# Performance work log

Hardware: AMD Instinct MI355X
Metric: run time of the kernel (lower is better)

Reference implementation:

```python
import jax, jax.numpy as jnp
import numpy as np

DIM = 1024
NUM_HEADS = 16
HEAD_DIM = DIM // NUM_HEADS


def setup_inputs() -> dict:
    key = jax.random.key(0)
    k_x, k_q, k_k, k_v, k_o = jax.random.split(key, 5)
    B, L = 2, 2048
    scale = 1.0 / np.sqrt(DIM)
    x_bld = jax.random.normal(k_x, (B, L, DIM), dtype=jnp.float32)
    # LinearGeneral kernels: (in_features, num_heads, head_dim) for q/k/v,
    # (num_heads, head_dim, out_features) for out. Init ~ lecun_normal-ish scale.
    Wq = jax.random.normal(k_q, (DIM, NUM_HEADS, HEAD_DIM), dtype=jnp.float32) * scale
    Wk = jax.random.normal(k_k, (DIM, NUM_HEADS, HEAD_DIM), dtype=jnp.float32) * scale
    Wv = jax.random.normal(k_v, (DIM, NUM_HEADS, HEAD_DIM), dtype=jnp.float32) * scale
    Wo = jax.random.normal(k_o, (NUM_HEADS, HEAD_DIM, DIM), dtype=jnp.float32) * scale
    return {"x_bld": x_bld, "Wq": Wq, "Wk": Wk, "Wv": Wv, "Wo": Wo}


def reference(x_bld, Wq, Wk, Wv, Wo) -> jnp.ndarray:
    # Projections: [B,L,D] x [D,H,hd] -> [B,L,H,hd]
    q_blhd = jnp.einsum('bld,dhk->blhk', x_bld, Wq)
    k_blhd = jnp.einsum('bld,dhk->blhk', x_bld, Wk)
    v_blhd = jnp.einsum('bld,dhk->blhk', x_bld, Wv)
    # Scores: [B,H,L,L]
    attn_bhll = jnp.einsum('bqhd,bkhd->bhqk', q_blhd, k_blhd)
    attn_bhll = attn_bhll / jnp.sqrt(jnp.asarray(HEAD_DIM, dtype=attn_bhll.dtype))
    L = x_bld.shape[1]
    qi = jnp.arange(L)[:, None]
    ki = jnp.arange(L)[None, :]
    mask_ll = ki <= qi  # causal, no window
    neg_inf = jnp.finfo(attn_bhll.dtype).min
    attn_bhll = jnp.where(mask_ll[None, None, :, :], attn_bhll, neg_inf)
    attn_bhll = jax.nn.softmax(attn_bhll, axis=-1)
    y_blhd = jnp.einsum('bhqk,bkhd->bqhd', attn_bhll, v_blhd)
    # Output projection: contract (H, hd) -> D
    return jnp.einsum('blhk,hkd->bld', y_blhd, Wo)
```

## Files before the change

kernel.cpp:

```cpp
#include <hip/hip_runtime.h>
#include <hip/hip_bf16.h>

typedef __hip_bfloat16 bf16;
typedef __attribute__((ext_vector_type(8))) short short8;
typedef __attribute__((ext_vector_type(4))) float f32x4;
typedef __attribute__((ext_vector_type(4))) unsigned int u32x4;

__device__ __forceinline__ float bfbits2f(unsigned short u) {
    return __uint_as_float(((unsigned int)u) << 16);
}
__device__ __forceinline__ unsigned short f2bfbits(float f) {
    union { float f; unsigned int u; } x;
    x.f = f;
    unsigned int r = x.u + 0x7FFFu + ((x.u >> 16) & 1u);
    return (unsigned short)(r >> 16);
}
__device__ __forceinline__ unsigned int pack_bf16x2(float lo, float hi) {
    unsigned int u0 = __float_as_uint(lo) + 0x8000u;
    unsigned int u1 = __float_as_uint(hi) + 0x8000u;
    return __builtin_amdgcn_perm(u1, u0, 0x07060302u);
}
__device__ __forceinline__ void async_copy16(const void* g, void* l) {
    __builtin_amdgcn_global_load_lds(
        (const __attribute__((address_space(1))) void*)g,
        (__attribute__((address_space(3))) void*)l, 16, 0, 0);
}
__device__ __forceinline__ bool sniff_bf16(const unsigned int* p, int lane) {
    unsigned int wd = p[lane];
    unsigned int e = (wd >> 7) & 0xFFu;
    return __popcll(__ballot(e >= 90u && e <= 150u)) > 40;
}

__global__ __launch_bounds__(256) void prep(
    const void* __restrict__ X, const void* __restrict__ W1,
    const void* __restrict__ W2, const void* __restrict__ W3,
    const void* __restrict__ W4, short* __restrict__ xb,
    short* __restrict__ O1, short* __restrict__ O2,
    short* __restrict__ O3, short* __restrict__ O4) {
    __shared__ float tbuf[32][33];
    const int bx = blockIdx.x;
    const int tid = threadIdx.x;
    const int lane = tid & 63;

    if (bx < 2048) {
        const bool isBf = sniff_bf16((const unsigned int*)X, lane);
        const int i = (bx * 256 + tid) * 8;
        if (isBf) {
            *(short8*)&xb[i] = *(const short8*)((const short*)X + i);
        } else {
            const float* xf = (const float*)X + i;
            float4 a = *(const float4*)xf;
            float4 b = *(const float4*)(xf + 4);
            short8 o;
            o[0] = (short)f2bfbits(a.x); o[1] = (short)f2bfbits(a.y);
            o[2] = (short)f2bfbits(a.z); o[3] = (short)f2bfbits(a.w);
            o[4] = (short)f2bfbits(b.x); o[5] = (short)f2bfbits(b.y);
            o[6] = (short)f2bfbits(b.z); o[7] = (short)f2bfbits(b.w);
            *(short8*)&xb[i] = o;
        }
    } else {
        const void* Ws[4] = {W1, W2, W3, W4};
        short* Os[4] = {O1, O2, O3, O4};
        const int t = bx - 2048;
        const int wsel = t >> 10;
        const int tile = t & 1023;
        const int bxt = tile & 31, byt = tile >> 5;
        const void* W = Ws[wsel];
        const bool isBf = sniff_bf16((const unsigned int*)W, lane);
        const float scale = (wsel == 0) ? 0.18033688f : 1.0f;
        short* O = Os[wsel];

        const int tx = tid & 31, ty = tid >> 5;
        const int gx = bxt * 32 + tx;
#pragma unroll
        for (int i = 0; i < 4; i++) {
            const int gy = byt * 32 + ty + i * 8;
            float v = isBf
                ? bfbits2f(((const unsigned short*)W)[(size_t)gy * 1024 + gx])
                : ((const float*)W)[(size_t)gy * 1024 + gx];
            tbuf[ty + i * 8][tx] = v * scale;
        }
        __syncthreads();
#pragma unroll
        for (int i = 0; i < 4; i++) {
            const int orow = bxt * 32 + ty + i * 8;
            const int ocol = byt * 32 + tx;
            O[(size_t)orow * 1024 + ocol] = (short)f2bfbits(tbuf[tx][ty + i * 8]);
        }
    }
}

template <int BN>
__global__ __launch_bounds__(256) void gemm_async(const short* __restrict__ A,
                                                  const short* __restrict__ Bt,
                                                  void* __restrict__ C,
                                                  const unsigned int* __restrict__ xdet,
                                                  short* __restrict__ VtGp,
                                                  int M, int N, int K) {
    __shared__ short As[2][128 * 32];
    __shared__ short Bs[2][BN * 32];
    constexpr int NI = BN / 32;

    const int tid = threadIdx.x;
    const int lane = tid & 63;
    const int wv = __builtin_amdgcn_readfirstlane(tid >> 6);
    const int quad = lane >> 4, l16 = lane & 15;
    const int wr = wv >> 1, wc = wv & 1;
    const int m0 = blockIdx.y * 128, n0 = blockIdx.x * BN;

    const int gr = lane >> 2;
    const int gc = ((lane & 3) ^ ((lane >> 3) & 3)) * 8;

    const f32x4 zero = {0.f, 0.f, 0.f, 0.f};
    f32x4 acc[4][NI];
#pragma unroll
    for (int mi = 0; mi < 4; mi++)
#pragma unroll
        for (int ni = 0; ni < NI; ni++) acc[mi][ni] = zero;

    const short* aptr[2];
    const short* bptr[BN / 64];
#pragma unroll
    for (int t = 0; t < 2; t++)
        aptr[t] = A + (size_t)(m0 + t * 64 + wv * 16 + gr) * K + gc;
#pragma unroll
    for (int t = 0; t < BN / 64; t++)
        bptr[t] = Bt + (size_t)(n0 + t * 64 + wv * 16 + gr) * K + gc;

#pragma unroll
    for (int t = 0; t < 2; t++) async_copy16(aptr[t], &As[0][(t * 64 + wv * 16) * 32]);
#pragma unroll
    for (int t = 0; t < BN / 64; t++) async_copy16(bptr[t], &Bs[0][(t * 64 + wv * 16) * 32]);

    const int ss = (quad ^ ((l16 >> 1) & 3)) * 8;

    for (int k0 = 0; k0 < K; k0 += 32) {
        const int cur = (k0 >> 5) & 1;
        __syncthreads();
        if (k0 + 32 < K) {
            const int nxt = cur ^ 1;
#pragma unroll
            for (int t = 0; t < 2; t++)
                async_copy16(aptr[t] + k0 + 32, &As[nxt][(t * 64 + wv * 16) * 32]);
#pragma unroll
            for (int t = 0; t < BN / 64; t++)
                async_copy16(bptr[t] + k0 + 32, &Bs[nxt][(t * 64 + wv * 16) * 32]);
        }

        short8 af[4], bfv[NI];
#pragma unroll
        for (int mi = 0; mi < 4; mi++)
            af[mi] = *(const short8*)&As[cur][(wr * 64 + mi * 16 + l16) * 32 + ss];
#pragma unroll
        for (int ni = 0; ni < NI; ni++)
            bfv[ni] = *(const short8*)&Bs[cur][(wc * (BN / 2) + ni * 16 + l16) * 32 + ss];
#pragma unroll
        for (int mi = 0; mi < 4; mi++)
#pragma unroll
            for (int ni = 0; ni < NI; ni++)
                acc[mi][ni] = __builtin_amdgcn_mfma_f32_16x16x32_bf16(
                    af[mi], bfv[ni], acc[mi][ni], 0, 0, 0);
    }

    if (VtGp != nullptr && n0 >= 2048) {
        unsigned short* Vw = (unsigned short*)VtGp;
#pragma unroll
        for (int mi = 0; mi < 4; mi++)
#pragma unroll
            for (int ni = 0; ni < NI; ni++)
#pragma unroll
                for (int r = 0; r < 4; r++) {
                    const int row = m0 + wr * 64 + mi * 16 + quad * 4 + r;
                    const int col = n0 + wc * (BN / 2) + ni * 16 + l16;
                    const int vcol = col - 2048;
                    const int hh = vcol >> 6, d = vcol & 63;
                    const int bb = row >> 11, lloc = row & 2047;
                    const int pl = (lloc & ~31) + 2 * (lloc & 15) + ((lloc >> 4) & 1);
                    Vw[((size_t)(bb * 16 + hh) * 64 + d) * 2048 + pl] =
                        f2bfbits(acc[mi][ni][r]);
                }
        return;
    }

    bool outBf = true;
    if (xdet) outBf = sniff_bf16(xdet, lane);
    if (outBf) {
        unsigned short* Cb = (unsigned short*)C;
#pragma unroll
        for (int mi = 0; mi < 4; mi++)
#pragma unroll
            for (int ni = 0; ni < NI; ni++)
#pragma unroll
                for (int r = 0; r < 4; r++) {
                    const int row = m0 + wr * 64 + mi * 16 + quad * 4 + r;
                    const int col = n0 + wc * (BN / 2) + ni * 16 + l16;
                    Cb[(size_t)row * N + col] = f2bfbits(acc[mi][ni][r]);
                }
    } else {
        float* Cf = (float*)C;
#pragma unroll
        for (int mi = 0; mi < 4; mi++)
#pragma unroll
            for (int ni = 0; ni < NI; ni++)
#pragma unroll
                for (int r = 0; r < 4; r++) {
                    const int row = m0 + wr * 64 + mi * 16 + quad * 4 + r;
                    const int col = n0 + wc * (BN / 2) + ni * 16 + l16;
                    Cf[(size_t)row * N + col] = acc[mi][ni][r];
                }
    }
}

__global__ __launch_bounds__(256) void attn_mfma9(
    const short* __restrict__ qkv, const short* __restrict__ VtG,
    short* __restrict__ Yg, short* __restrict__ Opart, float* __restrict__ ml) {
    __shared__ short Ks[2][64 * 64];
    __shared__ short Vt[2][64 * 64];
    __shared__ float scr[16][68];
    __shared__ float lred[2][64];

    const int tid = threadIdx.x;
    const int lane = tid & 63;
    const int wv = __builtin_amdgcn_readfirstlane(tid >> 6);
    const int wvq = wv >> 1, wvk = wv & 1;
    const int quad = lane >> 4, l16 = lane & 15;
    const int bh = blockIdx.x;
    const int b = bh >> 4, h = bh & 15;

    int qb, seg, S;
    const int slot = blockIdx.y;
    if (slot < 64)      { qb = 31 - (slot >> 2); seg = slot & 3; S = 4; }
    else if (slot < 80) { const int t2 = slot - 64; qb = 15 - (t2 >> 1); seg = t2 & 1; S = 2; }
    else                { qb = 87 - slot; seg = 0; S = 1; }

    const int ns = qb + 1;
    const int sb0 = seg * ns / S;
    const int sb1 = (seg + 1) * ns / S;

    const int rr = lane >> 3;
    const int scol = ((lane & 7) ^ rr) * 8;

    const short* kptr[2];
    const short* vptr[2];
    short* kdst[2];
    short* vdst[2];
#pragma unroll
    for (int i = 0; i < 2; i++) {
        const int u = wv * 2 + i;
        kptr[i] = qkv + (size_t)(b * 2048 + sb0 * 64 + u * 8 + rr) * 3072 + 1024 +
                  h * 64 + scol;
        kdst[i] = &Ks[0][(u * 8) * 64];
        vptr[i] = VtG + ((size_t)bh * 64 + u * 8 + rr) * 2048 + sb0 * 64 + scol;
        vdst[i] = &Vt[0][(u * 8) * 64];
    }
    const int bufoff = 64 * 64;
    const int buf0 = sb0 & 1;

#pragma unroll
    for (int i = 0; i < 2; i++) {
        async_copy16(kptr[i], kdst[i] + buf0 * bufoff);
        async_copy16(vptr[i], vdst[i] + buf0 * bufoff);
        kptr[i] += 64 * 3072;
        vptr[i] += 64;
    }
    short8 qf[2][2];
    {
        const short* qbase = qkv + (size_t)(b * 2048 + qb * 64 + wvq * 32 + l16) * 3072 +
                             h * 64 + quad * 8;
#pragma unroll
        for (int qt = 0; qt < 2; qt++)
#pragma unroll
            for (int hf = 0; hf < 2; hf++)
                qf[qt][hf] = *(const short8*)(qbase + qt * 16 * 3072 + hf * 32);
    }
    __syncthreads();

    const int sl = (quad ^ (l16 & 7)) * 8;

    const f32x4 minit = {-17.3123405f, -17.3123405f, -17.3123405f, -17.3123405f};
    f32x4 O[2][4];
#pragma unroll
    for (int qt = 0; qt < 2; qt++)
#pragma unroll
        for (int dt = 0; dt < 4; dt++) O[qt][dt] = {0.f, 0.f, 0.f, 0.f};
    float lp[2] = {0.f, 0.f};
    const int keyA0 = wvk * 32 + quad * 4;

    for (int sb = sb0; sb < sb1; sb++) {
        const int cur = sb & 1;
        if (sb != sb0) __syncthreads();
        if (sb + 1 < sb1) {
            const int nxt = cur ^ 1;
#pragma unroll
            for (int i = 0; i < 2; i++) {
                async_copy16(kptr[i], kdst[i] + nxt * bufoff);
                async_copy16(vptr[i], vdst[i] + nxt * bufoff);
                kptr[i] += 64 * 3072;
                vptr[i] += 64;
            }
        }
        const short* Kc = &Ks[cur][0];
        const short* Vc = &Vt[cur][0];

        short8 kf[2][2], vf[4];
#pragma unroll
        for (int kt = 0; kt < 2; kt++)
#pragma unroll
            for (int hf = 0; hf < 2; hf++)
                kf[kt][hf] = *(const short8*)
                    &Kc[(wvk * 32 + kt * 16 + l16) * 64 + (sl ^ (hf << 5))];
#pragma unroll
        for (int dt = 0; dt < 4; dt++)
            vf[dt] = *(const short8*)
                &Vc[(dt * 16 + l16) * 64 + (sl ^ (wvk << 5))];

#pragma unroll
        for (int qt = 0; qt < 2; qt++) {
            f32x4 sA = __builtin_amdgcn_mfma_f32_16x16x32_bf16(kf[0][0], qf[qt][0], minit, 0, 0, 0);
            sA = __builtin_amdgcn_mfma_f32_16x16x32_bf16(kf[0][1], qf[qt][1], sA, 0, 0, 0);
            f32x4 sB = __builtin_amdgcn_mfma_f32_16x16x32_bf16(kf[1][0], qf[qt][0], minit, 0, 0, 0);
            sB = __builtin_amdgcn_mfma_f32_16x16x32_bf16(kf[1][1], qf[qt][1], sB, 0, 0, 0);
            if (sb == qb) {
                const int qcol = wvq * 32 + qt * 16 + l16;
#pragma unroll
                for (int r = 0; r < 4; r++) {
                    if (keyA0 + r > qcol) sA[r] = -1e30f;
                    if (keyA0 + 16 + r > qcol) sB[r] = -1e30f;
                }
            }
            union { u32x4 u; short8 s; } pa;
#pragma unroll
            for (int t = 0; t < 4; t++) {
                sA[t] = __builtin_amdgcn_exp2f(sA[t]);
                sB[t] = __builtin_amdgcn_exp2f(sB[t]);
                lp[qt] += sA[t] + sB[t];
                pa.u[t] = pack_bf16x2(sA[t], sB[t]);
            }
#pragma unroll
            for (int dt = 0; dt < 4; dt++)
                O[qt][dt] = __builtin_amdgcn_mfma_f32_16x16x32_bf16(
                    pa.s, vf[dt], O[qt][dt], 0, 0, 0);
        }
    }

#pragma unroll
    for (int qt = 0; qt < 2; qt++) {
        float v = lp[qt];
        v += __shfl_xor(v, 16);
        v += __shfl_xor(v, 32);
        if (quad == 0) lred[wvk][wvq * 32 + qt * 16 + l16] = v;
    }

#pragma unroll
    for (int g = 0; g < 2; g++)
#pragma unroll
        for (int qt = 0; qt < 2; qt++) {
            __syncthreads();
            if (wvq == g && wvk == 1) {
#pragma unroll
                for (int dt = 0; dt < 4; dt++)
#pragma unroll
                    for (int r = 0; r < 4; r++)
                        scr[quad * 4 + r][dt * 16 + l16] = O[qt][dt][r];
            }
            __syncthreads();
            if (wvq == g && wvk == 0) {
#pragma unroll
                for (int dt = 0; dt < 4; dt++)
#pragma unroll
                    for (int r = 0; r < 4; r++)
                        O[qt][dt][r] += scr[quad * 4 + r][dt * 16 + l16];
            }
        }

    if (wvk == 0) {
        if (S == 1) {
#pragma unroll
            for (int qt = 0; qt < 2; qt++)
#pragma unroll
                for (int r = 0; r < 4; r++) {
                    const int q = wvq * 32 + qt * 16 + quad * 4 + r;
                    const float inv = 1.f / (lred[0][q] + lred[1][q]);
#pragma unroll
                    for (int dt = 0; dt < 4; dt++)
                        Yg[(size_t)(b * 2048 + qb * 64 + q) * 1024 + h * 64 +
                           dt * 16 + l16] = (short)f2bfbits(O[qt][dt][r] * inv);
                }
        } else {
            const int qidx = qb - 8;
            const int base = ((seg * 32 + bh) * 24 + qidx) * 64;
#pragma unroll
            for (int qt = 0; qt < 2; qt++)
#pragma unroll
                for (int r = 0; r < 4; r++) {
                    const int q = wvq * 32 + qt * 16 + quad * 4 + r;
#pragma unroll
                    for (int dt = 0; dt < 4; dt++)
                        Opart[(size_t)(base + q) * 64 + dt * 16 + l16] =
                            (short)f2bfbits(O[qt][dt][r]);
                    if (l16 == 0) ml[base + q] = lred[0][q] + lred[1][q];
                }
        }
    }
}

__global__ __launch_bounds__(256) void attn_combine6(
    const short* __restrict__ Opart, const float* __restrict__ ml,
    short* __restrict__ Yg) {
    const int qb = 8 + blockIdx.x;
    const int bh = blockIdx.y;
    const int b = bh >> 4, h = bh & 15;
    const int S = (qb >= 16) ? 4 : 2;
    const int qidx = qb - 8;
    const int tid = threadIdx.x;
    const int q = tid >> 2;
    const int d0 = (tid & 3) * 16;

    float a0[8] = {}, a1[8] = {};
    float lsum = 0.f;
    for (int s = 0; s < S; s++) {
        const int idx = ((s * 32 + bh) * 24 + qidx) * 64 + q;
        lsum += ml[idx];
        const short* p = Opart + (size_t)idx * 64 + d0;
        short8 x0 = *(const short8*)p;
        short8 x1 = *(const short8*)(p + 8);
#pragma unroll
        for (int t = 0; t < 8; t++) {
            a0[t] += bfbits2f((unsigned short)x0[t]);
            a1[t] += bfbits2f((unsigned short)x1[t]);
        }
    }
    const float inv = 1.f / lsum;
    short8 o0, o1;
#pragma unroll
    for (int t = 0; t < 8; t++) {
        o0[t] = (short)f2bfbits(a0[t] * inv);
        o1[t] = (short)f2bfbits(a1[t] * inv);
    }
    short* yp = Yg + (size_t)(b * 2048 + qb * 64 + q) * 1024 + h * 64 + d0;
    *(short8*)yp = o0;
    *(short8*)(yp + 8) = o1;
}

extern "C" void kernel_launch(void* const* d_in, const int* in_sizes, int n_in,
                              void* d_out, int out_size, void* d_ws, size_t ws_size,
                              hipStream_t stream) {
    const int M = 2 * 2048;
    const int D = 1024;

    char* w = (char*)d_ws;
    short* xb  = (short*)w;
    short* WqT = (short*)(w + (8u << 20));
    short* WkT = WqT + (1u << 20);
    short* WvT = WkT + (1u << 20);
    short* WoT = WvT + (1u << 20);
    short* qkv = WoT + (1u << 20);
    short* VtG = qkv + (size_t)M * 3072;
    short* Opart = VtG + (size_t)2048 * 2048;
    float* mlp = (float*)(Opart + (size_t)4 * 32 * 24 * 64 * 64);
    short* y = xb;

    prep<<<6144, 256, 0, stream>>>(d_in[0], d_in[1], d_in[2], d_in[3], d_in[4],
                                   xb, WqT, WkT, WvT, WoT);

    gemm_async<128><<<dim3(3072 / 128, M / 128), 256, 0, stream>>>(
        xb, WqT, qkv, nullptr, VtG, M, 3072, D);

    attn_mfma9<<<dim3(32, 88), 256, 0, stream>>>(qkv, VtG, y, Opart, mlp);
    attn_combine6<<<dim3(24, 32), 256, 0, stream>>>(Opart, mlp, y);

    gemm_async<64><<<dim3(D / 64, M / 128), 256, 0, stream>>>(
        y, WoT, d_out, (const unsigned int*)d_in[0], nullptr, M, D, D);
}
```

Before: 180.8 us.

## Enlarge attention query tile to 128 rows, one 32-query slice per wave

The attention kernel now processes 128-query blocks, and each of the four waves owns 32 queries across all 64 keys of a tile. Previously the waves split along keys and had to reduce partial outputs through shared memory. This doubles reuse of each K/V tile loaded into LDS and removes the cross-wave O reduction with its barriers. It also adds per-wave causal masking over two diagonal tiles, s_setprio around the PV MFMAs, and a launch-bounds occupancy hint. The trade-off is fewer blocks (44 slots instead of 88) and some wasted masked work on diagonal tiles.

```diff
diff --git a/kernel.cpp b/kernel.cpp
--- a/kernel.cpp
+++ b/kernel.cpp
@@ -211,29 +211,27 @@
     }
 }
 
-__global__ __launch_bounds__(256) void attn_mfma9(
+__global__ __launch_bounds__(256, 4) void attn_mfma12(
     const short* __restrict__ qkv, const short* __restrict__ VtG,
     short* __restrict__ Yg, short* __restrict__ Opart, float* __restrict__ ml) {
     __shared__ short Ks[2][64 * 64];
     __shared__ short Vt[2][64 * 64];
-    __shared__ float scr[16][68];
-    __shared__ float lred[2][64];
+    __shared__ float lred[4][32];
 
     const int tid = threadIdx.x;
     const int lane = tid & 63;
     const int wv = __builtin_amdgcn_readfirstlane(tid >> 6);
-    const int wvq = wv >> 1, wvk = wv & 1;
     const int quad = lane >> 4, l16 = lane & 15;
     const int bh = blockIdx.x;
     const int b = bh >> 4, h = bh & 15;
 
-    int qb, seg, S;
+    int qbb, seg, S;
     const int slot = blockIdx.y;
-    if (slot < 64)      { qb = 31 - (slot >> 2); seg = slot & 3; S = 4; }
-    else if (slot < 80) { const int t2 = slot - 64; qb = 15 - (t2 >> 1); seg = t2 & 1; S = 2; }
-    else                { qb = 87 - slot; seg = 0; S = 1; }
-
-    const int ns = qb + 1;
+    if (slot < 32)      { qbb = 15 - (slot >> 2); seg = slot & 3; S = 4; }
+    else if (slot < 40) { const int t2 = slot - 32; qbb = 7 - (t2 >> 1); seg = t2 & 1; S = 2; }
+    else                { qbb = 43 - slot; seg = 0; S = 1; }
+
+    const int ns = 2 * qbb + 2;
     const int sb0 = seg * ns / S;
     const int sb1 = (seg + 1) * ns / S;
 
@@ -265,8 +263,8 @@
     }
     short8 qf[2][2];
     {
-        const short* qbase = qkv + (size_t)(b * 2048 + qb * 64 + wvq * 32 + l16) * 3072 +
-                             h * 64 + quad * 8;
+        const short* qbase = qkv +
+            (size_t)(b * 2048 + qbb * 128 + wv * 32 + l16) * 3072 + h * 64 + quad * 8;
 #pragma unroll
         for (int qt = 0; qt < 2; qt++)
 #pragma unroll
@@ -284,7 +282,7 @@
 #pragma unroll
         for (int dt = 0; dt < 4; dt++) O[qt][dt] = {0.f, 0.f, 0.f, 0.f};
     float lp[2] = {0.f, 0.f};
-    const int keyA0 = wvk * 32 + quad * 4;
+    const int qmin = qbb * 128 + wv * 32;
 
     for (int sb = sb0; sb < sb1; sb++) {
         const int cur = sb & 1;
@@ -301,45 +299,53 @@
         }
         const short* Kc = &Ks[cur][0];
         const short* Vc = &Vt[cur][0];
-
-        short8 kf[2][2], vf[4];
-#pragma unroll
-        for (int kt = 0; kt < 2; kt++)
-#pragma unroll
-            for (int hf = 0; hf < 2; hf++)
-                kf[kt][hf] = *(const short8*)
-                    &Kc[(wvk * 32 + kt * 16 + l16) * 64 + (sl ^ (hf << 5))];
-#pragma unroll
-        for (int dt = 0; dt < 4; dt++)
-            vf[dt] = *(const short8*)
-                &Vc[(dt * 16 + l16) * 64 + (sl ^ (wvk << 5))];
-
-#pragma unroll
-        for (int qt = 0; qt < 2; qt++) {
-            f32x4 sA = __builtin_amdgcn_mfma_f32_16x16x32_bf16(kf[0][0], qf[qt][0], minit, 0, 0, 0);
-            sA = __builtin_amdgcn_mfma_f32_16x16x32_bf16(kf[0][1], qf[qt][1], sA, 0, 0, 0);
-            f32x4 sB = __builtin_amdgcn_mfma_f32_16x16x32_bf16(kf[1][0], qf[qt][0], minit, 0, 0, 0);
-            sB = __builtin_amdgcn_mfma_f32_16x16x32_bf16(kf[1][1], qf[qt][1], sB, 0, 0, 0);
-            if (sb == qb) {
-                const int qcol = wvq * 32 + qt * 16 + l16;
-#pragma unroll
-                for (int r = 0; r < 4; r++) {
-                    if (keyA0 + r > qcol) sA[r] = -1e30f;
-                    if (keyA0 + 16 + r > qcol) sB[r] = -1e30f;
+        const bool needmask = (sb * 64 + 63 > qmin);
+
+#pragma unroll
+        for (int c = 0; c < 2; c++) {
+            short8 kf0[2], kf1[2], vf[4];
+#pragma unroll
+            for (int hf = 0; hf < 2; hf++) {
+                kf0[hf] = *(const short8*)
+                    &Kc[((2 * c) * 16 + l16) * 64 + (sl ^ (hf << 5))];
+                kf1[hf] = *(const short8*)
+                    &Kc[((2 * c + 1) * 16 + l16) * 64 + (sl ^ (hf << 5))];
+            }
+#pragma unroll
+            for (int dt = 0; dt < 4; dt++)
+                vf[dt] = *(const short8*)
+                    &Vc[(dt * 16 + l16) * 64 + (sl ^ (c << 5))];
+
+#pragma unroll
+            for (int qt = 0; qt < 2; qt++) {
+                f32x4 sA = __builtin_amdgcn_mfma_f32_16x16x32_bf16(kf0[0], qf[qt][0], minit, 0, 0, 0);
+                sA = __builtin_amdgcn_mfma_f32_16x16x32_bf16(kf0[1], qf[qt][1], sA, 0, 0, 0);
+                f32x4 sB = __builtin_amdgcn_mfma_f32_16x16x32_bf16(kf1[0], qf[qt][0], minit, 0, 0, 0);
+                sB = __builtin_amdgcn_mfma_f32_16x16x32_bf16(kf1[1], qf[qt][1], sB, 0, 0, 0);
+                if (needmask) {
+                    const int qcol = qmin + qt * 16 + l16;
+                    const int key0 = sb * 64 + c * 32 + quad * 4;
+#pragma unroll
+                    for (int r = 0; r < 4; r++) {
+                        if (key0 + r > qcol) sA[r] = -1e30f;
+                        if (key0 + 16 + r > qcol) sB[r] = -1e30f;
+                    }
                 }
+                union { u32x4 u; short8 s; } pa;
+#pragma unroll
+                for (int t = 0; t < 4; t++) {
+                    sA[t] = __builtin_amdgcn_exp2f(sA[t]);
+                    sB[t] = __builtin_amdgcn_exp2f(sB[t]);
+                    lp[qt] += sA[t] + sB[t];
+                    pa.u[t] = pack_bf16x2(sA[t], sB[t]);
+                }
+                __builtin_amdgcn_s_setprio(1);
+#pragma unroll
+                for (int dt = 0; dt < 4; dt++)
+                    O[qt][dt] = __builtin_amdgcn_mfma_f32_16x16x32_bf16(
+                        pa.s, vf[dt], O[qt][dt], 0, 0, 0);
+                __builtin_amdgcn_s_setprio(0);
             }
-            union { u32x4 u; short8 s; } pa;
-#pragma unroll
-            for (int t = 0; t < 4; t++) {
-                sA[t] = __builtin_amdgcn_exp2f(sA[t]);
-                sB[t] = __builtin_amdgcn_exp2f(sB[t]);
-                lp[qt] += sA[t] + sB[t];
-                pa.u[t] = pack_bf16x2(sA[t], sB[t]);
-            }
-#pragma unroll
-            for (int dt = 0; dt < 4; dt++)
-                O[qt][dt] = __builtin_amdgcn_mfma_f32_16x16x32_bf16(
-                    pa.s, vf[dt], O[qt][dt], 0, 0, 0);
         }
     }
 
@@ -348,78 +354,56 @@
         float v = lp[qt];
         v += __shfl_xor(v, 16);
         v += __shfl_xor(v, 32);
-        if (quad == 0) lred[wvk][wvq * 32 + qt * 16 + l16] = v;
-    }
-
-#pragma unroll
-    for (int g = 0; g < 2; g++)
-#pragma unroll
-        for (int qt = 0; qt < 2; qt++) {
-            __syncthreads();
-            if (wvq == g && wvk == 1) {
+        if (quad == 0) lred[wv][qt * 16 + l16] = v;
+    }
+
+    if (S == 1) {
+#pragma unroll
+        for (int qt = 0; qt < 2; qt++)
+#pragma unroll
+            for (int r = 0; r < 4; r++) {
+                const int q = wv * 32 + qt * 16 + quad * 4 + r;
+                const float inv = 1.f / lred[wv][qt * 16 + quad * 4 + r];
 #pragma unroll
                 for (int dt = 0; dt < 4; dt++)
-#pragma unroll
-                    for (int r = 0; r < 4; r++)
-                        scr[quad * 4 + r][dt * 16 + l16] = O[qt][dt][r];
+                    Yg[(size_t)(b * 2048 + qbb * 128 + q) * 1024 + h * 64 +
+                       dt * 16 + l16] = (short)f2bfbits(O[qt][dt][r] * inv);
             }
-            __syncthreads();
-            if (wvq == g && wvk == 0) {
+    } else {
+        const int qidx = qbb - 4;
+        const int base = ((seg * 32 + bh) * 12 + qidx) * 128;
+#pragma unroll
+        for (int qt = 0; qt < 2; qt++)
+#pragma unroll
+            for (int r = 0; r < 4; r++) {
+                const int q = wv * 32 + qt * 16 + quad * 4 + r;
 #pragma unroll
                 for (int dt = 0; dt < 4; dt++)
-#pragma unroll
-                    for (int r = 0; r < 4; r++)
-                        O[qt][dt][r] += scr[quad * 4 + r][dt * 16 + l16];
+                    Opart[(size_t)(base + q) * 64 + dt * 16 + l16] =
+                        (short)f2bfbits(O[qt][dt][r]);
+                if (l16 == 0) ml[base + q] = lred[wv][qt * 16 + quad * 4 + r];
             }
-        }
-
-    if (wvk == 0) {
-        if (S == 1) {
-#pragma unroll
-            for (int qt = 0; qt < 2; qt++)
-#pragma unroll
-                for (int r = 0; r < 4; r++) {
-                    const int q = wvq * 32 + qt * 16 + quad * 4 + r;
-                    const float inv = 1.f / (lred[0][q] + lred[1][q]);
-#pragma unroll
-                    for (int dt = 0; dt < 4; dt++)
-                        Yg[(size_t)(b * 2048 + qb * 64 + q) * 1024 + h * 64 +
-                           dt * 16 + l16] = (short)f2bfbits(O[qt][dt][r] * inv);
-                }
-        } else {
-            const int qidx = qb - 8;
-            const int base = ((seg * 32 + bh) * 24 + qidx) * 64;
-#pragma unroll
-            for (int qt = 0; qt < 2; qt++)
-#pragma unroll
-                for (int r = 0; r < 4; r++) {
-                    const int q = wvq * 32 + qt * 16 + quad * 4 + r;
-#pragma unroll
-                    for (int dt = 0; dt < 4; dt++)
-                        Opart[(size_t)(base + q) * 64 + dt * 16 + l16] =
-                            (short)f2bfbits(O[qt][dt][r]);
-                    if (l16 == 0) ml[base + q] = lred[0][q] + lred[1][q];
-                }
-        }
-    }
-}
-
-__global__ __launch_bounds__(256) void attn_combine6(
+    }
+}
+
+__global__ __launch_bounds__(256) void attn_combine11(
     const short* __restrict__ Opart, const float* __restrict__ ml,
     short* __restrict__ Yg) {
-    const int qb = 8 + blockIdx.x;
+    const int x = blockIdx.x;
+    const int qbb = 4 + (x >> 1);
+    const int half = x & 1;
     const int bh = blockIdx.y;
     const int b = bh >> 4, h = bh & 15;
-    const int S = (qb >= 16) ? 4 : 2;
-    const int qidx = qb - 8;
+    const int S = (qbb >= 8) ? 4 : 2;
+    const int qidx = qbb - 4;
     const int tid = threadIdx.x;
-    const int q = tid >> 2;
+    const int q = (tid >> 2) + half * 64;
     const int d0 = (tid & 3) * 16;
 
     float a0[8] = {}, a1[8] = {};
     float lsum = 0.f;
     for (int s = 0; s < S; s++) {
-        const int idx = ((s * 32 + bh) * 24 + qidx) * 64 + q;
+        const int idx = ((s * 32 + bh) * 12 + qidx) * 128 + q;
         lsum += ml[idx];
         const short* p = Opart + (size_t)idx * 64 + d0;
         short8 x0 = *(const short8*)p;
@@ -437,7 +421,7 @@
         o0[t] = (short)f2bfbits(a0[t] * inv);
         o1[t] = (short)f2bfbits(a1[t] * inv);
     }
-    short* yp = Yg + (size_t)(b * 2048 + qb * 64 + q) * 1024 + h * 64 + d0;
+    short* yp = Yg + (size_t)(b * 2048 + qbb * 128 + q) * 1024 + h * 64 + d0;
     *(short8*)yp = o0;
     *(short8*)(yp + 8) = o1;
 }
@@ -457,7 +441,7 @@
     short* qkv = WoT + (1u << 20);
     short* VtG = qkv + (size_t)M * 3072;
     short* Opart = VtG + (size_t)2048 * 2048;
-    float* mlp = (float*)(Opart + (size_t)4 * 32 * 24 * 64 * 64);
+    float* mlp = (float*)(Opart + (size_t)4 * 32 * 12 * 128 * 64);
     short* y = xb;
 
     prep<<<6144, 256, 0, stream>>>(d_in[0], d_in[1], d_in[2], d_in[3], d_in[4],
@@ -466,8 +450,8 @@
     gemm_async<128><<<dim3(3072 / 128, M / 128), 256, 0, stream>>>(
         xb, WqT, qkv, nullptr, VtG, M, 3072, D);
 
-    attn_mfma9<<<dim3(32, 88), 256, 0, stream>>>(qkv, VtG, y, Opart, mlp);
-    attn_combine6<<<dim3(24, 32), 256, 0, stream>>>(Opart, mlp, y);
+    attn_mfma12<<<dim3(32, 44), 256, 0, stream>>>(qkv, VtG, y, Opart, mlp);
+    attn_combine11<<<dim3(24, 32), 256, 0, stream>>>(Opart, mlp, y);
 
     gemm_async<64><<<dim3(D / 64, M / 128), 256, 0, stream>>>(
         y, WoT, d_out, (const unsigned int*)d_in[0], nullptr, M, D, D);
```

Measured after the change: 180.5 us. No clear change (-0.2%).
